# Performance work log

Measured on AMD Instinct MI355X. Metric: run time of the kernel, lower is better.

The kernel has to match this reference:

```python
import jax, jax.numpy as jnp
import numpy as np

DIM = 256
CODEBOOK_SIZE = 1024

def setup_inputs() -> dict:
    key = jax.random.key(0)
    kx, ke = jax.random.split(key)
    x = jax.random.normal(kx, (32, 2048, DIM), dtype=jnp.float32)
    embed = jax.random.normal(ke, (CODEBOOK_SIZE, DIM), dtype=jnp.float32)
    return {"x": x, "embed": embed}

def reference(x, embed):
    # Eval-mode forward of EuclideanCodebook (training=False: no EMA / dropout / dead-code replace).
    d = x.shape[-1]
    flatten = x.reshape(-1, d)                                   # (N, d)
    dist = ((flatten ** 2).sum(axis=1, keepdims=True)
            - 2.0 * flatten @ embed.T
            + (embed ** 2).sum(axis=1)[None, :])                 # (N, K)
    embed_ind = jnp.argmin(dist, axis=-1)                        # (N,)
    quantize = jnp.take(embed, embed_ind, axis=0)                # (N, d)
    residual = jax.lax.stop_gradient(quantize) - jax.lax.stop_gradient(flatten)
    return quantize, embed_ind, residual
```

## Files before the change

### kernel.cpp

```cpp
#include <hip/hip_runtime.h>
#include <math.h>
#include <float.h>

#define DIM 256
#define MARGIN 0.125f
#define EPS_TIE 1e-4
#define PREFER_LOWER 1

#define BMB 128

typedef __attribute__((ext_vector_type(8))) short short8;
typedef __attribute__((ext_vector_type(4))) float f32x4;

__device__ __forceinline__ unsigned short f32_to_bf16_rne(float f) {
    unsigned int u = __float_as_uint(f);
    u += 0x7fffu + ((u >> 16) & 1u);
    return (unsigned short)(u >> 16);
}
__device__ __forceinline__ float bf16_to_f32(unsigned short h) {
    return __uint_as_float((unsigned int)h << 16);
}

__global__ void esq_kernel(const float* __restrict__ embed, float* __restrict__ esq) {
    const int j = blockIdx.x;
    const int lane = threadIdx.x;
    float4 v = *reinterpret_cast<const float4*>(embed + (size_t)j * DIM + lane * 4);
    float s = v.x * v.x + v.y * v.y + v.z * v.z + v.w * v.w;
#pragma unroll
    for (int m = 32; m >= 1; m >>= 1) s += __shfl_xor(s, m, 64);
    if (lane == 0) esq[j] = s;
}

__global__ void efrag_kernel(const float* __restrict__ embed,
                             unsigned short* __restrict__ ehi,
                             unsigned short* __restrict__ elo) {
    const int b = blockIdx.x;
    const int l = threadIdx.x;
    const int ct = b >> 3, s = b & 7;
    const int col = ct * 16 + (l & 15);
    const int kb  = s * 32 + (l >> 4) * 8;
    const float* src = embed + (size_t)col * DIM + kb;
    float4 v0 = *reinterpret_cast<const float4*>(src);
    float4 v1 = *reinterpret_cast<const float4*>(src + 4);
    float vv[8] = {v0.x, v0.y, v0.z, v0.w, v1.x, v1.y, v1.z, v1.w};
    unsigned short hh[8], ll[8];
#pragma unroll
    for (int i = 0; i < 8; ++i) {
        unsigned short h = f32_to_bf16_rne(vv[i]);
        hh[i] = h;
        ll[i] = f32_to_bf16_rne(vv[i] - bf16_to_f32(h));
    }
    size_t base = ((size_t)b * 64 + l) * 8;
#pragma unroll
    for (int i = 0; i < 8; ++i) { ehi[base + i] = hh[i]; elo[base + i] = ll[i]; }
}

__global__ __launch_bounds__(256, 2)
void vq_mfma_kernel(const float* __restrict__ x, const float* __restrict__ embed,
                    const unsigned short* __restrict__ ehi,
                    const unsigned short* __restrict__ elo,
                    const float* __restrict__ esq, float* __restrict__ out,
                    int N, int K) {
    __shared__ float  esq_lds[1024];
    __shared__ double rv1[256], rv2[256];
    __shared__ int    ri1[256], ri2[256];
    __shared__ float  xrow[DIM];
    __shared__ int    flr[BMB];
    __shared__ int    nflag;

    const int t = threadIdx.x;
    const int w = t >> 6;
    const int l = t & 63;
    const int ar = l & 15;
    const int ag = l >> 4;
    const int row0  = blockIdx.x * BMB;
    const int wrow0 = row0 + w * 32;

    if (t == 0) nflag = 0;
    for (int i = t; i < 1024; i += 256) esq_lds[i] = esq[i];

    short8 ahi[2][8], alo[2][8];
#pragma unroll
    for (int rt = 0; rt < 2; ++rt)
#pragma unroll
        for (int s = 0; s < 8; ++s) {
            const float* src = x + (size_t)(wrow0 + rt * 16 + ar) * DIM + s * 32 + ag * 8;
            float4 v0 = *reinterpret_cast<const float4*>(src);
            float4 v1 = *reinterpret_cast<const float4*>(src + 4);
            float vv[8] = {v0.x, v0.y, v0.z, v0.w, v1.x, v1.y, v1.z, v1.w};
#pragma unroll
            for (int i = 0; i < 8; ++i) {
                unsigned short h = f32_to_bf16_rne(vv[i]);
                ahi[rt][s][i] = (short)h;
                alo[rt][s][i] = (short)f32_to_bf16_rne(vv[i] - bf16_to_f32(h));
            }
        }
    __syncthreads();

    float minv[8], min2v[8]; int mini[8];
#pragma unroll
    for (int i = 0; i < 8; ++i) { minv[i] = INFINITY; min2v[i] = INFINITY; mini[i] = 0; }

    for (int jc = 0; jc < 16; ++jc) {
        f32x4 acc[2][4];
#pragma unroll
        for (int rt = 0; rt < 2; ++rt)
#pragma unroll
            for (int ct = 0; ct < 4; ++ct) acc[rt][ct] = (f32x4)0.0f;

#pragma unroll
        for (int s = 0; s < 8; ++s) {
            short8 bhi[4], blo[4];
#pragma unroll
            for (int ct = 0; ct < 4; ++ct) {
                size_t base = (((size_t)(jc * 4 + ct) * 8 + s) * 64 + l) * 8;
                bhi[ct] = *reinterpret_cast<const short8*>(ehi + base);
                blo[ct] = *reinterpret_cast<const short8*>(elo + base);
            }
#pragma unroll
            for (int rt = 0; rt < 2; ++rt)
#pragma unroll
                for (int ct = 0; ct < 4; ++ct) {
                    acc[rt][ct] = __builtin_amdgcn_mfma_f32_16x16x32_bf16(
                        ahi[rt][s], bhi[ct], acc[rt][ct], 0, 0, 0);
                    acc[rt][ct] = __builtin_amdgcn_mfma_f32_16x16x32_bf16(
                        ahi[rt][s], blo[ct], acc[rt][ct], 0, 0, 0);
                    acc[rt][ct] = __builtin_amdgcn_mfma_f32_16x16x32_bf16(
                        alo[rt][s], bhi[ct], acc[rt][ct], 0, 0, 0);
                }
        }
#pragma unroll
        for (int rt = 0; rt < 2; ++rt)
#pragma unroll
            for (int ct = 0; ct < 4; ++ct) {
                int col = jc * 64 + ct * 16 + ar;
                float eq = esq_lds[col];
#pragma unroll
                for (int r = 0; r < 4; ++r) {
                    float sc = fmaf(-2.0f, acc[rt][ct][r], eq);
                    int ii = rt * 4 + r;
                    if (sc < minv[ii]) { min2v[ii] = minv[ii]; minv[ii] = sc; mini[ii] = col; }
                    else if (sc < min2v[ii]) { min2v[ii] = sc; }
                }
            }
    }

#pragma unroll
    for (int ii = 0; ii < 8; ++ii) {
        float v1 = minv[ii]; int i1 = mini[ii]; float v2 = min2v[ii];
#pragma unroll
        for (int m = 1; m < 16; m <<= 1) {
            float ov1 = __shfl_xor(v1, m, 64);
            int   oi1 = __shfl_xor(i1, m, 64);
            float ov2 = __shfl_xor(v2, m, 64);
            float nv2 = fminf(fmaxf(v1, ov1), fminf(v2, ov2));
            if (ov1 < v1 || (ov1 == v1 && oi1 < i1)) { v1 = ov1; i1 = oi1; }
            v2 = nv2;
        }
        minv[ii] = v1; mini[ii] = i1; min2v[ii] = v2;
    }

    const size_t IOFF = (size_t)N * DIM;
    const size_t ROFF = IOFF + (size_t)N;
#pragma unroll
    for (int ii = 0; ii < 8; ++ii) {
        const int rt = ii >> 2, r = ii & 3;
        const int row = wrow0 + rt * 16 + ag * 4 + r;
        const int idx = mini[ii];
        if (ar == 0) {
            out[IOFF + row] = (float)idx;
            if (min2v[ii] - minv[ii] < MARGIN) {
                int p = atomicAdd(&nflag, 1);
                flr[p] = row - row0;
            }
        }
#pragma unroll
        for (int q = 0; q < 4; ++q) {
            int d0 = ar * 16 + q * 4;
            float4 e  = *reinterpret_cast<const float4*>(embed + (size_t)idx * DIM + d0);
            float4 xv = *reinterpret_cast<const float4*>(x + (size_t)row * DIM + d0);
            *reinterpret_cast<float4*>(out + (size_t)row * DIM + d0) = e;
            float4 rr = make_float4(e.x - xv.x, e.y - xv.y, e.z - xv.z, e.w - xv.w);
            *reinterpret_cast<float4*>(out + ROFF + (size_t)row * DIM + d0) = rr;
        }
    }

    __syncthreads();
    const int nf = nflag;
    for (int f = 0; f < nf; ++f) {
        const int row = row0 + flr[f];
        if (t < 64) {
            float4 v = *reinterpret_cast<const float4*>(x + (size_t)row * DIM + t * 4);
            xrow[t * 4 + 0] = v.x; xrow[t * 4 + 1] = v.y;
            xrow[t * 4 + 2] = v.z; xrow[t * 4 + 3] = v.w;
        }
        __syncthreads();

        double v1 = DBL_MAX, v2 = DBL_MAX; int i1 = 0x7fffffff, i2 = 0x7fffffff;
#pragma unroll
        for (int jj = 0; jj < 4; ++jj) {
            const int j = t * 4 + jj;
            const float* e = embed + (size_t)j * DIM;
            double xe = 0.0, ee = 0.0;
            for (int kg = 0; kg < DIM / 4; ++kg) {
                float4 ev = *reinterpret_cast<const float4*>(e + kg * 4);
                double e0 = ev.x, e1 = ev.y, e2 = ev.z, e3 = ev.w;
                xe += e0 * (double)xrow[kg * 4 + 0] + e1 * (double)xrow[kg * 4 + 1]
                    + e2 * (double)xrow[kg * 4 + 2] + e3 * (double)xrow[kg * 4 + 3];
                ee += e0 * e0 + e1 * e1 + e2 * e2 + e3 * e3;
            }
            double d = ee - 2.0 * xe;
            if (d < v1 || (d == v1 && j < i1)) { v2 = v1; i2 = i1; v1 = d; i1 = j; }
            else if (d < v2 || (d == v2 && j < i2)) { v2 = d; i2 = j; }
        }
        rv1[t] = v1; ri1[t] = i1; rv2[t] = v2; ri2[t] = i2;
        __syncthreads();
        for (int s = 128; s > 0; s >>= 1) {
            if (t < s) {
                double a1 = rv1[t],     a2 = rv2[t];     int k1 = ri1[t],     k2 = ri2[t];
                double b1 = rv1[t + s], b2 = rv2[t + s]; int j1 = ri1[t + s], j2 = ri2[t + s];
                double w1, w2; int m1, m2;
                bool bfirst = (b1 < a1) || (b1 == a1 && j1 < k1);
                if (bfirst) {
                    w1 = b1; m1 = j1;
                    if (a1 < b2 || (a1 == b2 && k1 < j2)) { w2 = a1; m2 = k1; }
                    else                                   { w2 = b2; m2 = j2; }
                } else {
                    w1 = a1; m1 = k1;
                    if (b1 < a2 || (b1 == a2 && j1 < k2)) { w2 = b1; m2 = j1; }
                    else                                   { w2 = a2; m2 = k2; }
                }
                rv1[t] = w1; ri1[t] = m1; rv2[t] = w2; ri2[t] = m2;
            }
            __syncthreads();
        }
        int idx = ri1[0];
        {
            const double gap = rv2[0] - rv1[0];
#if PREFER_LOWER
            if (gap < EPS_TIE && ri2[0] < ri1[0]) idx = ri2[0];
#else
            if (gap < EPS_TIE && ri2[0] > ri1[0]) idx = ri2[0];
#endif
        }
        if (t == 0) out[IOFF + row] = (float)idx;
        if (t < 64) {
            int d0 = t * 4;
            float4 e  = *reinterpret_cast<const float4*>(embed + (size_t)idx * DIM + d0);
            float4 xv = *reinterpret_cast<const float4*>(x + (size_t)row * DIM + d0);
            *reinterpret_cast<float4*>(out + (size_t)row * DIM + d0) = e;
            float4 rr = make_float4(e.x - xv.x, e.y - xv.y, e.z - xv.z, e.w - xv.w);
            *reinterpret_cast<float4*>(out + ROFF + (size_t)row * DIM + d0) = rr;
        }
        __syncthreads();
    }
}

#define BM 64
#define BN 64
#define DK 64
__global__ __launch_bounds__(256, 4)
void vq_argmin_kernel(const float* __restrict__ x, const float* __restrict__ embed,
                      const float* __restrict__ esq, float* __restrict__ out,
                      int N, int K) {
    __shared__ float xs[DK][BM];
    __shared__ float es[DK][BN];
    __shared__ double rv1[256], rv2[256];
    __shared__ int    ri1[256], ri2[256];
    __shared__ float  xrow[DIM];
    __shared__ int    flr[BM];
    __shared__ int    nflag;

    const int t = threadIdx.x;
    const int tx = t & 15, ty = t >> 4;
    const int row0 = blockIdx.x * BM;
    if (t == 0) nflag = 0;

    float minv[4], min2v[4]; int mini[4];
#pragma unroll
    for (int r = 0; r < 4; ++r) { minv[r] = INFINITY; min2v[r] = INFINITY; mini[r] = 0; }

    for (int jc = 0; jc < K / BN; ++jc) {
        float acc[4][4];
#pragma unroll
        for (int r = 0; r < 4; ++r)
#pragma unroll
            for (int c = 0; c < 4; ++c) acc[r][c] = 0.0f;
        for (int dc = 0; dc < DIM / DK; ++dc) {
            __syncthreads();
#pragma unroll
            for (int it = 0; it < 4; ++it) {
                int idx = t + 256 * it, r = idx & 63, kg = idx >> 6;
                float4 v = *reinterpret_cast<const float4*>(
                    x + (size_t)(row0 + r) * DIM + dc * DK + kg * 4);
                xs[kg*4+0][r] = v.x; xs[kg*4+1][r] = v.y; xs[kg*4+2][r] = v.z; xs[kg*4+3][r] = v.w;
            }
#pragma unroll
            for (int it = 0; it < 4; ++it) {
                int idx = t + 256 * it, c = idx & 63, kg = idx >> 6;
                float4 v = *reinterpret_cast<const float4*>(
                    embed + (size_t)(jc * BN + c) * DIM + dc * DK + kg * 4);
                es[kg*4+0][c] = v.x; es[kg*4+1][c] = v.y; es[kg*4+2][c] = v.z; es[kg*4+3][c] = v.w;
            }
            __syncthreads();
#pragma unroll
            for (int k = 0; k < DK; ++k) {
                float4 a = *reinterpret_cast<const float4*>(&xs[k][ty * 4]);
                float4 b = *reinterpret_cast<const float4*>(&es[k][tx * 4]);
                float arr[4] = {a.x, a.y, a.z, a.w}, bc[4] = {b.x, b.y, b.z, b.w};
#pragma unroll
                for (int r = 0; r < 4; ++r)
#pragma unroll
                    for (int c = 0; c < 4; ++c) acc[r][c] = fmaf(arr[r], bc[c], acc[r][c]);
            }
        }
        float4 eq = *reinterpret_cast<const float4*>(esq + jc * BN + tx * 4);
        float eqa[4] = {eq.x, eq.y, eq.z, eq.w};
#pragma unroll
        for (int c = 0; c < 4; ++c) {
            int j = jc * BN + tx * 4 + c;
#pragma unroll
            for (int r = 0; r < 4; ++r) {
                float s = fmaf(-2.0f, acc[r][c], eqa[c]);
                if (s < minv[r]) { min2v[r] = minv[r]; minv[r] = s; mini[r] = j; }
                else if (s < min2v[r]) { min2v[r] = s; }
            }
        }
    }
#pragma unroll
    for (int r = 0; r < 4; ++r) {
        float v1 = minv[r]; int i1 = mini[r]; float v2 = min2v[r];
#pragma unroll
        for (int m = 1; m < 16; m <<= 1) {
            float ov1 = __shfl_xor(v1, m, 64); int oi1 = __shfl_xor(i1, m, 64);
            float ov2 = __shfl_xor(v2, m, 64);
            float nv2 = fminf(fmaxf(v1, ov1), fminf(v2, ov2));
            if (ov1 < v1 || (ov1 == v1 && oi1 < i1)) { v1 = ov1; i1 = oi1; }
            v2 = nv2;
        }
        minv[r] = v1; mini[r] = i1; min2v[r] = v2;
    }
    const size_t IOFF = (size_t)N * DIM, ROFF = IOFF + (size_t)N;
#pragma unroll
    for (int r = 0; r < 4; ++r) {
        int row = row0 + ty * 4 + r, idx = mini[r];
        if (tx == 0) {
            out[IOFF + row] = (float)idx;
            if (min2v[r] - minv[r] < MARGIN) { int p = atomicAdd(&nflag, 1); flr[p] = ty * 4 + r; }
        }
#pragma unroll
        for (int g = 0; g < 4; ++g) {
            int d0 = tx * 16 + g * 4;
            float4 e  = *reinterpret_cast<const float4*>(embed + (size_t)idx * DIM + d0);
            float4 xv = *reinterpret_cast<const float4*>(x + (size_t)row * DIM + d0);
            *reinterpret_cast<float4*>(out + (size_t)row * DIM + d0) = e;
            float4 rr = make_float4(e.x - xv.x, e.y - xv.y, e.z - xv.z, e.w - xv.w);
            *reinterpret_cast<float4*>(out + ROFF + (size_t)row * DIM + d0) = rr;
        }
    }
    __syncthreads();
    const int nf = nflag;
    for (int f = 0; f < nf; ++f) {
        const int row = row0 + flr[f];
        if (t < 64) {
            float4 v = *reinterpret_cast<const float4*>(x + (size_t)row * DIM + t * 4);
            xrow[t*4+0] = v.x; xrow[t*4+1] = v.y; xrow[t*4+2] = v.z; xrow[t*4+3] = v.w;
        }
        __syncthreads();
        double v1 = DBL_MAX, v2 = DBL_MAX; int i1 = 0x7fffffff, i2 = 0x7fffffff;
#pragma unroll
        for (int jj = 0; jj < 4; ++jj) {
            const int j = t * 4 + jj;
            const float* e = embed + (size_t)j * DIM;
            double xe = 0.0, ee = 0.0;
            for (int kg = 0; kg < DIM / 4; ++kg) {
                float4 ev = *reinterpret_cast<const float4*>(e + kg * 4);
                double e0 = ev.x, e1 = ev.y, e2 = ev.z, e3 = ev.w;
                xe += e0*(double)xrow[kg*4+0] + e1*(double)xrow[kg*4+1]
                    + e2*(double)xrow[kg*4+2] + e3*(double)xrow[kg*4+3];
                ee += e0*e0 + e1*e1 + e2*e2 + e3*e3;
            }
            double d = ee - 2.0 * xe;
            if (d < v1 || (d == v1 && j < i1)) { v2 = v1; i2 = i1; v1 = d; i1 = j; }
            else if (d < v2 || (d == v2 && j < i2)) { v2 = d; i2 = j; }
        }
        rv1[t] = v1; ri1[t] = i1; rv2[t] = v2; ri2[t] = i2;
        __syncthreads();
        for (int s = 128; s > 0; s >>= 1) {
            if (t < s) {
                double a1 = rv1[t], a2 = rv2[t]; int k1 = ri1[t], k2 = ri2[t];
                double b1 = rv1[t+s], b2 = rv2[t+s]; int j1 = ri1[t+s], j2 = ri2[t+s];
                double w1, w2; int m1, m2;
                bool bfirst = (b1 < a1) || (b1 == a1 && j1 < k1);
                if (bfirst) { w1 = b1; m1 = j1;
                    if (a1 < b2 || (a1 == b2 && k1 < j2)) { w2 = a1; m2 = k1; } else { w2 = b2; m2 = j2; }
                } else { w1 = a1; m1 = k1;
                    if (b1 < a2 || (b1 == a2 && j1 < k2)) { w2 = b1; m2 = j1; } else { w2 = a2; m2 = k2; }
                }
                rv1[t] = w1; ri1[t] = m1; rv2[t] = w2; ri2[t] = m2;
            }
            __syncthreads();
        }
        int idx = ri1[0];
        const double gap = rv2[0] - rv1[0];
#if PREFER_LOWER
        if (gap < EPS_TIE && ri2[0] < ri1[0]) idx = ri2[0];
#else
        if (gap < EPS_TIE && ri2[0] > ri1[0]) idx = ri2[0];
#endif
        if (t == 0) out[IOFF + row] = (float)idx;
        if (t < 64) {
            int d0 = t * 4;
            float4 e  = *reinterpret_cast<const float4*>(embed + (size_t)idx * DIM + d0);
            float4 xv = *reinterpret_cast<const float4*>(x + (size_t)row * DIM + d0);
            *reinterpret_cast<float4*>(out + (size_t)row * DIM + d0) = e;
            float4 rr = make_float4(e.x - xv.x, e.y - xv.y, e.z - xv.z, e.w - xv.w);
            *reinterpret_cast<float4*>(out + ROFF + (size_t)row * DIM + d0) = rr;
        }
        __syncthreads();
    }
}

extern "C" void kernel_launch(void* const* d_in, const int* in_sizes, int n_in,
                              void* d_out, int out_size, void* d_ws, size_t ws_size,
                              hipStream_t stream) {
    const float* x     = (const float*)d_in[0];
    const float* embed = (const float*)d_in[1];
    float* out = (float*)d_out;
    const int N = in_sizes[0] / DIM;
    const int K = in_sizes[1] / DIM;

    float* esq = (float*)d_ws;
    unsigned short* ehi = (unsigned short*)((char*)d_ws + 4096);
    unsigned short* elo = (unsigned short*)((char*)d_ws + 4096 + 524288);
    const size_t need = 4096 + 2 * 524288;

    esq_kernel<<<K, 64, 0, stream>>>(embed, esq);
    if (ws_size >= need) {
        efrag_kernel<<<(K / 16) * 8, 64, 0, stream>>>(embed, ehi, elo);
        vq_mfma_kernel<<<N / BMB, 256, 0, stream>>>(x, embed, ehi, elo, esq, out, N, K);
    } else {
        vq_argmin_kernel<<<N / BM, 256, 0, stream>>>(x, embed, esq, out, N, K);
    }
}
```

Baseline: 436.8 us.

## Split codebook columns across waves with LDS-staged double-buffered B fragments

Each block now handles 32 rows instead of 128. All four waves share those rows, and each wave owns a 16-column slice of every 64-column chunk. Codebook bf16 fragments are staged into LDS with async global_load_lds, double-buffered against the MFMA work. Per-wave argmin results are merged through shared memory, and the gather/residual write is re-laid out as coalesced full-row float4 accesses. This cuts per-wave accumulator registers and raises the occupancy target, but adds a __syncthreads per k-step and makes every block re-read the whole codebook for only 32 rows, four times as many codebook passes overall.

Result: slower. 727.0 us (+66.5%).

```diff
diff --git a/kernel.cpp b/kernel.cpp
--- a/kernel.cpp
+++ b/kernel.cpp
@@ -7,7 +7,7 @@
 #define EPS_TIE 1e-4
 #define PREFER_LOWER 1
 
-#define BMB 128
+#define ROWS 32
 
 typedef __attribute__((ext_vector_type(8))) short short8;
 typedef __attribute__((ext_vector_type(4))) float f32x4;
@@ -19,6 +19,13 @@
 }
 __device__ __forceinline__ float bf16_to_f32(unsigned short h) {
     return __uint_as_float((unsigned int)h << 16);
+}
+
+__device__ __forceinline__ void stage16(const void* gsrc, void* ldst) {
+    __builtin_amdgcn_global_load_lds(
+        (const __attribute__((address_space(1))) unsigned int*)gsrc,
+        (__attribute__((address_space(3))) unsigned int*)ldst,
+        16, 0, 0);
 }
 
 __global__ void esq_kernel(const float* __restrict__ embed, float* __restrict__ esq) {
@@ -55,26 +62,29 @@
     for (int i = 0; i < 8; ++i) { ehi[base + i] = hh[i]; elo[base + i] = ll[i]; }
 }
 
-__global__ __launch_bounds__(256, 2)
+__global__ __launch_bounds__(256, 3)
 void vq_mfma_kernel(const float* __restrict__ x, const float* __restrict__ embed,
                     const unsigned short* __restrict__ ehi,
                     const unsigned short* __restrict__ elo,
                     const float* __restrict__ esq, float* __restrict__ out,
                     int N, int K) {
+    __shared__ unsigned short bfrag[2][4][2][512];
     __shared__ float  esq_lds[1024];
+    __shared__ float  mv1[4][ROWS], mv2[4][ROWS];
+    __shared__ int    mi1[4][ROWS];
+    __shared__ int    rowidx[ROWS];
     __shared__ double rv1[256], rv2[256];
     __shared__ int    ri1[256], ri2[256];
     __shared__ float  xrow[DIM];
-    __shared__ int    flr[BMB];
+    __shared__ int    flr[ROWS];
     __shared__ int    nflag;
 
-    const int t = threadIdx.x;
-    const int w = t >> 6;
-    const int l = t & 63;
+    const int t  = threadIdx.x;
+    const int w  = t >> 6;
+    const int l  = t & 63;
     const int ar = l & 15;
     const int ag = l >> 4;
-    const int row0  = blockIdx.x * BMB;
-    const int wrow0 = row0 + w * 32;
+    const int row0 = blockIdx.x * ROWS;
 
     if (t == 0) nflag = 0;
     for (int i = t; i < 1024; i += 256) esq_lds[i] = esq[i];
@@ -84,7 +94,7 @@
     for (int rt = 0; rt < 2; ++rt)
 #pragma unroll
         for (int s = 0; s < 8; ++s) {
-            const float* src = x + (size_t)(wrow0 + rt * 16 + ar) * DIM + s * 32 + ag * 8;
+            const float* src = x + (size_t)(row0 + rt * 16 + ar) * DIM + s * 32 + ag * 8;
             float4 v0 = *reinterpret_cast<const float4*>(src);
             float4 v1 = *reinterpret_cast<const float4*>(src + 4);
             float vv[8] = {v0.x, v0.y, v0.z, v0.w, v1.x, v1.y, v1.z, v1.w};
@@ -95,55 +105,56 @@
                 alo[rt][s][i] = (short)f32_to_bf16_rne(vv[i] - bf16_to_f32(h));
             }
         }
+
+#define STAGE(CB, JC, S) do {                                                   \
+        size_t go_ = (((size_t)((JC) * 4 + w) * 8 + (S)) * 64 + l) * 8;         \
+        stage16(ehi + go_, &bfrag[CB][w][0][0]);                                \
+        stage16(elo + go_, &bfrag[CB][w][1][0]);                                \
+    } while (0)
+
+    STAGE(0, 0, 0);
     __syncthreads();
 
     float minv[8], min2v[8]; int mini[8];
 #pragma unroll
     for (int i = 0; i < 8; ++i) { minv[i] = INFINITY; min2v[i] = INFINITY; mini[i] = 0; }
 
+    f32x4 acc0 = (f32x4)0.0f, acc1 = (f32x4)0.0f;
+
     for (int jc = 0; jc < 16; ++jc) {
-        f32x4 acc[2][4];
-#pragma unroll
-        for (int rt = 0; rt < 2; ++rt)
-#pragma unroll
-            for (int ct = 0; ct < 4; ++ct) acc[rt][ct] = (f32x4)0.0f;
-
 #pragma unroll
         for (int s = 0; s < 8; ++s) {
-            short8 bhi[4], blo[4];
-#pragma unroll
-            for (int ct = 0; ct < 4; ++ct) {
-                size_t base = (((size_t)(jc * 4 + ct) * 8 + s) * 64 + l) * 8;
-                bhi[ct] = *reinterpret_cast<const short8*>(ehi + base);
-                blo[ct] = *reinterpret_cast<const short8*>(elo + base);
-            }
-#pragma unroll
-            for (int rt = 0; rt < 2; ++rt)
-#pragma unroll
-                for (int ct = 0; ct < 4; ++ct) {
-                    acc[rt][ct] = __builtin_amdgcn_mfma_f32_16x16x32_bf16(
-                        ahi[rt][s], bhi[ct], acc[rt][ct], 0, 0, 0);
-                    acc[rt][ct] = __builtin_amdgcn_mfma_f32_16x16x32_bf16(
-                        ahi[rt][s], blo[ct], acc[rt][ct], 0, 0, 0);
-                    acc[rt][ct] = __builtin_amdgcn_mfma_f32_16x16x32_bf16(
-                        alo[rt][s], bhi[ct], acc[rt][ct], 0, 0, 0);
-                }
-        }
-#pragma unroll
-        for (int rt = 0; rt < 2; ++rt)
-#pragma unroll
-            for (int ct = 0; ct < 4; ++ct) {
-                int col = jc * 64 + ct * 16 + ar;
-                float eq = esq_lds[col];
-#pragma unroll
-                for (int r = 0; r < 4; ++r) {
-                    float sc = fmaf(-2.0f, acc[rt][ct][r], eq);
-                    int ii = rt * 4 + r;
-                    if (sc < minv[ii]) { min2v[ii] = minv[ii]; minv[ii] = sc; mini[ii] = col; }
-                    else if (sc < min2v[ii]) { min2v[ii] = sc; }
-                }
-            }
-    }
+            const int cb = s & 1;
+            if (s < 7)            STAGE(cb ^ 1, jc, s + 1);
+            else if (jc < 15)     STAGE(cb ^ 1, jc + 1, 0);
+            short8 bh = *reinterpret_cast<const short8*>(&bfrag[cb][w][0][l * 8]);
+            short8 bl = *reinterpret_cast<const short8*>(&bfrag[cb][w][1][l * 8]);
+            acc0 = __builtin_amdgcn_mfma_f32_16x16x32_bf16(ahi[0][s], bh, acc0, 0, 0, 0);
+            acc0 = __builtin_amdgcn_mfma_f32_16x16x32_bf16(ahi[0][s], bl, acc0, 0, 0, 0);
+            acc0 = __builtin_amdgcn_mfma_f32_16x16x32_bf16(alo[0][s], bh, acc0, 0, 0, 0);
+            acc1 = __builtin_amdgcn_mfma_f32_16x16x32_bf16(ahi[1][s], bh, acc1, 0, 0, 0);
+            acc1 = __builtin_amdgcn_mfma_f32_16x16x32_bf16(ahi[1][s], bl, acc1, 0, 0, 0);
+            acc1 = __builtin_amdgcn_mfma_f32_16x16x32_bf16(alo[1][s], bh, acc1, 0, 0, 0);
+            __syncthreads();
+        }
+        const int col = jc * 64 + w * 16 + ar;
+        const float eq = esq_lds[col];
+#pragma unroll
+        for (int r = 0; r < 4; ++r) {
+            float sc = fmaf(-2.0f, acc0[r], eq);
+            if (sc < minv[r]) { min2v[r] = minv[r]; minv[r] = sc; mini[r] = col; }
+            else if (sc < min2v[r]) min2v[r] = sc;
+        }
+#pragma unroll
+        for (int r = 0; r < 4; ++r) {
+            float sc = fmaf(-2.0f, acc1[r], eq);
+            int ii = 4 + r;
+            if (sc < minv[ii]) { min2v[ii] = minv[ii]; minv[ii] = sc; mini[ii] = col; }
+            else if (sc < min2v[ii]) min2v[ii] = sc;
+        }
+        acc0 = (f32x4)0.0f; acc1 = (f32x4)0.0f;
+    }
+#undef STAGE
 
 #pragma unroll
     for (int ii = 0; ii < 8; ++ii) {
@@ -159,30 +170,44 @@
         }
         minv[ii] = v1; mini[ii] = i1; min2v[ii] = v2;
     }
+    if (ar == 0) {
+#pragma unroll
+        for (int ii = 0; ii < 8; ++ii) {
+            int rr = (ii >> 2) * 16 + ag * 4 + (ii & 3);
+            mv1[w][rr] = minv[ii]; mi1[w][rr] = mini[ii]; mv2[w][rr] = min2v[ii];
+        }
+    }
+    __syncthreads();
+    if (t < ROWS) {
+        float v1 = mv1[0][t]; int i1 = mi1[0][t]; float v2 = mv2[0][t];
+#pragma unroll
+        for (int ww = 1; ww < 4; ++ww) {
+            float ov1 = mv1[ww][t]; int oi1 = mi1[ww][t]; float ov2 = mv2[ww][t];
+            float nv2 = fminf(fmaxf(v1, ov1), fminf(v2, ov2));
+            if (ov1 < v1 || (ov1 == v1 && oi1 < i1)) { v1 = ov1; i1 = oi1; }
+            v2 = nv2;
+        }
+        rowidx[t] = i1;
+        if (v2 - v1 < MARGIN) {
+            int p = atomicAdd(&nflag, 1);
+            flr[p] = t;
+        }
+    }
+    __syncthreads();
 
     const size_t IOFF = (size_t)N * DIM;
     const size_t ROFF = IOFF + (size_t)N;
 #pragma unroll
-    for (int ii = 0; ii < 8; ++ii) {
-        const int rt = ii >> 2, r = ii & 3;
-        const int row = wrow0 + rt * 16 + ag * 4 + r;
-        const int idx = mini[ii];
-        if (ar == 0) {
-            out[IOFF + row] = (float)idx;
-            if (min2v[ii] - minv[ii] < MARGIN) {
-                int p = atomicAdd(&nflag, 1);
-                flr[p] = row - row0;
-            }
-        }
-#pragma unroll
-        for (int q = 0; q < 4; ++q) {
-            int d0 = ar * 16 + q * 4;
-            float4 e  = *reinterpret_cast<const float4*>(embed + (size_t)idx * DIM + d0);
-            float4 xv = *reinterpret_cast<const float4*>(x + (size_t)row * DIM + d0);
-            *reinterpret_cast<float4*>(out + (size_t)row * DIM + d0) = e;
-            float4 rr = make_float4(e.x - xv.x, e.y - xv.y, e.z - xv.z, e.w - xv.w);
-            *reinterpret_cast<float4*>(out + ROFF + (size_t)row * DIM + d0) = rr;
-        }
+    for (int rg = 0; rg < 8; ++rg) {
+        const int rr  = rg * 4 + w;
+        const int row = row0 + rr;
+        const int idx = rowidx[rr];
+        if (l == 0) out[IOFF + row] = (float)idx;
+        float4 e  = *reinterpret_cast<const float4*>(embed + (size_t)idx * DIM + l * 4);
+        float4 xv = *reinterpret_cast<const float4*>(x + (size_t)row * DIM + l * 4);
+        *reinterpret_cast<float4*>(out + (size_t)row * DIM + l * 4) = e;
+        float4 rv = make_float4(e.x - xv.x, e.y - xv.y, e.z - xv.z, e.w - xv.w);
+        *reinterpret_cast<float4*>(out + ROFF + (size_t)row * DIM + l * 4) = rv;
     }
 
     __syncthreads();
@@ -438,7 +463,7 @@
     esq_kernel<<<K, 64, 0, stream>>>(embed, esq);
     if (ws_size >= need) {
         efrag_kernel<<<(K / 16) * 8, 64, 0, stream>>>(embed, ehi, elo);
-        vq_mfma_kernel<<<N / BMB, 256, 0, stream>>>(x, embed, ehi, elo, esq, out, N, K);
+        vq_mfma_kernel<<<N / ROWS, 256, 0, stream>>>(x, embed, ehi, elo, esq, out, N, K);
     } else {
         vq_argmin_kernel<<<N / BM, 256, 0, stream>>>(x, embed, esq, out, N, K);
     }
```

## Stage codebook fragments via double-buffered LDS and use nontemporal streaming I/O

Applied to the files above, without the earlier changes.

Before this change, each wave loaded all four B fragment tiles from global memory, so all four waves fetched the same data. Now each wave loads one tile into a double-buffered LDS slot using global_load_lds, the four waves share those tiles, and the next s-step is prefetched while MFMAs run on the current one. The cost is a __syncthreads per s-step, 128 per block, which adds barrier stalls. The x reads and the quantize/residual writes now use nontemporal loads and stores to reduce cache pollution.

New measurement: 582.5 us. +33.3%, slower.

```diff
diff --git a/kernel.cpp b/kernel.cpp
--- a/kernel.cpp
+++ b/kernel.cpp
@@ -7,7 +7,7 @@
 #define EPS_TIE 1e-4
 #define PREFER_LOWER 1
 
-#define BMB 128
+#define ROWS 128
 
 typedef __attribute__((ext_vector_type(8))) short short8;
 typedef __attribute__((ext_vector_type(4))) float f32x4;
@@ -19,6 +19,20 @@
 }
 __device__ __forceinline__ float bf16_to_f32(unsigned short h) {
     return __uint_as_float((unsigned int)h << 16);
+}
+
+__device__ __forceinline__ f32x4 nt_load4(const float* p) {
+    return __builtin_nontemporal_load((const f32x4*)p);
+}
+__device__ __forceinline__ void nt_store4(float* p, f32x4 v) {
+    __builtin_nontemporal_store(v, (f32x4*)p);
+}
+
+__device__ __forceinline__ void stage16(const void* gsrc, void* ldst) {
+    __builtin_amdgcn_global_load_lds(
+        (const __attribute__((address_space(1))) unsigned int*)gsrc,
+        (__attribute__((address_space(3))) unsigned int*)ldst,
+        16, 0, 0);
 }
 
 __global__ void esq_kernel(const float* __restrict__ embed, float* __restrict__ esq) {
@@ -61,19 +75,20 @@
                     const unsigned short* __restrict__ elo,
                     const float* __restrict__ esq, float* __restrict__ out,
                     int N, int K) {
+    __shared__ unsigned short bfrag[2][4][2][512];
     __shared__ float  esq_lds[1024];
     __shared__ double rv1[256], rv2[256];
     __shared__ int    ri1[256], ri2[256];
     __shared__ float  xrow[DIM];
-    __shared__ int    flr[BMB];
+    __shared__ int    flr[ROWS];
     __shared__ int    nflag;
 
-    const int t = threadIdx.x;
-    const int w = t >> 6;
-    const int l = t & 63;
+    const int t  = threadIdx.x;
+    const int w  = t >> 6;
+    const int l  = t & 63;
     const int ar = l & 15;
     const int ag = l >> 4;
-    const int row0  = blockIdx.x * BMB;
+    const int row0  = blockIdx.x * ROWS;
     const int wrow0 = row0 + w * 32;
 
     if (t == 0) nflag = 0;
@@ -85,9 +100,9 @@
 #pragma unroll
         for (int s = 0; s < 8; ++s) {
             const float* src = x + (size_t)(wrow0 + rt * 16 + ar) * DIM + s * 32 + ag * 8;
-            float4 v0 = *reinterpret_cast<const float4*>(src);
-            float4 v1 = *reinterpret_cast<const float4*>(src + 4);
-            float vv[8] = {v0.x, v0.y, v0.z, v0.w, v1.x, v1.y, v1.z, v1.w};
+            f32x4 v0 = nt_load4(src);
+            f32x4 v1 = nt_load4(src + 4);
+            float vv[8] = {v0[0], v0[1], v0[2], v0[3], v1[0], v1[1], v1[2], v1[3]};
 #pragma unroll
             for (int i = 0; i < 8; ++i) {
                 unsigned short h = f32_to_bf16_rne(vv[i]);
@@ -95,55 +110,68 @@
                 alo[rt][s][i] = (short)f32_to_bf16_rne(vv[i] - bf16_to_f32(h));
             }
         }
+
+#define STAGE(CB, JC, S) do {                                                   \
+        size_t go_ = (((size_t)((JC) * 4 + w) * 8 + (S)) * 64 + l) * 8;         \
+        stage16(ehi + go_, &bfrag[CB][w][0][0]);                                \
+        stage16(elo + go_, &bfrag[CB][w][1][0]);                                \
+    } while (0)
+
+    STAGE(0, 0, 0);
     __syncthreads();
 
     float minv[8], min2v[8]; int mini[8];
 #pragma unroll
     for (int i = 0; i < 8; ++i) { minv[i] = INFINITY; min2v[i] = INFINITY; mini[i] = 0; }
 
+    f32x4 acc[2][4];
+#pragma unroll
+    for (int rt = 0; rt < 2; ++rt)
+#pragma unroll
+        for (int ct = 0; ct < 4; ++ct) acc[rt][ct] = (f32x4)0.0f;
+
     for (int jc = 0; jc < 16; ++jc) {
-        f32x4 acc[2][4];
-#pragma unroll
-        for (int rt = 0; rt < 2; ++rt)
-#pragma unroll
-            for (int ct = 0; ct < 4; ++ct) acc[rt][ct] = (f32x4)0.0f;
-
 #pragma unroll
         for (int s = 0; s < 8; ++s) {
-            short8 bhi[4], blo[4];
+            const int cb = s & 1;
+            if (s < 7)            STAGE(cb ^ 1, jc, s + 1);
+            else if (jc < 15)     STAGE(cb ^ 1, jc + 1, 0);
+            short8 bh[4], bl[4];
 #pragma unroll
             for (int ct = 0; ct < 4; ++ct) {
-                size_t base = (((size_t)(jc * 4 + ct) * 8 + s) * 64 + l) * 8;
-                bhi[ct] = *reinterpret_cast<const short8*>(ehi + base);
-                blo[ct] = *reinterpret_cast<const short8*>(elo + base);
+                bh[ct] = *reinterpret_cast<const short8*>(&bfrag[cb][ct][0][l * 8]);
+                bl[ct] = *reinterpret_cast<const short8*>(&bfrag[cb][ct][1][l * 8]);
             }
 #pragma unroll
             for (int rt = 0; rt < 2; ++rt)
 #pragma unroll
                 for (int ct = 0; ct < 4; ++ct) {
                     acc[rt][ct] = __builtin_amdgcn_mfma_f32_16x16x32_bf16(
-                        ahi[rt][s], bhi[ct], acc[rt][ct], 0, 0, 0);
+                        ahi[rt][s], bh[ct], acc[rt][ct], 0, 0, 0);
                     acc[rt][ct] = __builtin_amdgcn_mfma_f32_16x16x32_bf16(
-                        ahi[rt][s], blo[ct], acc[rt][ct], 0, 0, 0);
+                        ahi[rt][s], bl[ct], acc[rt][ct], 0, 0, 0);
                     acc[rt][ct] = __builtin_amdgcn_mfma_f32_16x16x32_bf16(
-                        alo[rt][s], bhi[ct], acc[rt][ct], 0, 0, 0);
+                        alo[rt][s], bh[ct], acc[rt][ct], 0, 0, 0);
                 }
+            __syncthreads();
         }
 #pragma unroll
         for (int rt = 0; rt < 2; ++rt)
 #pragma unroll
             for (int ct = 0; ct < 4; ++ct) {
-                int col = jc * 64 + ct * 16 + ar;
-                float eq = esq_lds[col];
+                const int col = jc * 64 + ct * 16 + ar;
+                const float eq = esq_lds[col];
 #pragma unroll
                 for (int r = 0; r < 4; ++r) {
                     float sc = fmaf(-2.0f, acc[rt][ct][r], eq);
                     int ii = rt * 4 + r;
                     if (sc < minv[ii]) { min2v[ii] = minv[ii]; minv[ii] = sc; mini[ii] = col; }
-                    else if (sc < min2v[ii]) { min2v[ii] = sc; }
+                    else if (sc < min2v[ii]) min2v[ii] = sc;
                 }
-            }
-    }
+                acc[rt][ct] = (f32x4)0.0f;
+            }
+    }
+#undef STAGE
 
 #pragma unroll
     for (int ii = 0; ii < 8; ++ii) {
@@ -177,11 +205,10 @@
 #pragma unroll
         for (int q = 0; q < 4; ++q) {
             int d0 = ar * 16 + q * 4;
-            float4 e  = *reinterpret_cast<const float4*>(embed + (size_t)idx * DIM + d0);
-            float4 xv = *reinterpret_cast<const float4*>(x + (size_t)row * DIM + d0);
-            *reinterpret_cast<float4*>(out + (size_t)row * DIM + d0) = e;
-            float4 rr = make_float4(e.x - xv.x, e.y - xv.y, e.z - xv.z, e.w - xv.w);
-            *reinterpret_cast<float4*>(out + ROFF + (size_t)row * DIM + d0) = rr;
+            f32x4 e  = *reinterpret_cast<const f32x4*>(embed + (size_t)idx * DIM + d0);
+            f32x4 xv = nt_load4(x + (size_t)row * DIM + d0);
+            nt_store4(out + (size_t)row * DIM + d0, e);
+            nt_store4(out + ROFF + (size_t)row * DIM + d0, e - xv);
         }
     }
 
@@ -438,7 +465,7 @@
     esq_kernel<<<K, 64, 0, stream>>>(embed, esq);
     if (ws_size >= need) {
         efrag_kernel<<<(K / 16) * 8, 64, 0, stream>>>(embed, ehi, elo);
-        vq_mfma_kernel<<<N / BMB, 256, 0, stream>>>(x, embed, ehi, elo, esq, out, N, K);
+        vq_mfma_kernel<<<N / ROWS, 256, 0, stream>>>(x, embed, ehi, elo, esq, out, N, K);
     } else {
         vq_argmin_kernel<<<N / BM, 256, 0, stream>>>(x, embed, esq, out, N, K);
     }
```

## Use single-bf16 MFMA with split-codebook partial argmin and exact fallback merge

Applied to the files above, without the earlier changes.

Drops the three-term hi/lo bf16 split and computes distances with a single bf16 MFMA per tile. The codebook is split into two halves held in registers across 512-row blocks, with x fragments staged in LDS. Per-half top-2 partial results go to a workspace, and a separate merge kernel picks the winner. The merge kernel flags close calls with wider margins for exact fp64 recomputation, and writes quantize and residual with nontemporal stores. This removes about two thirds of the MFMA work and the lo-fragment loads. The cost is more rows sent to the slow exact fallback, plus an extra kernel launch and workspace traffic.

Result: slower. 1.524 ms (+248.9%).

```diff
diff --git a/kernel.cpp b/kernel.cpp
--- a/kernel.cpp
+++ b/kernel.cpp
@@ -3,11 +3,11 @@
 #include <float.h>
 
 #define DIM 256
-#define MARGIN 0.125f
 #define EPS_TIE 1e-4
 #define PREFER_LOWER 1
-
-#define BMB 128
+#define MARGIN_MERGE 0.75f
+#define MARGIN_HALF  0.30f
+#define MARGIN_FALLBACK 0.125f
 
 typedef __attribute__((ext_vector_type(8))) short short8;
 typedef __attribute__((ext_vector_type(4))) float f32x4;
@@ -17,8 +17,8 @@
     u += 0x7fffu + ((u >> 16) & 1u);
     return (unsigned short)(u >> 16);
 }
-__device__ __forceinline__ float bf16_to_f32(unsigned short h) {
-    return __uint_as_float((unsigned int)h << 16);
+__device__ __forceinline__ void nt_store4(float* p, f32x4 v) {
+    __builtin_nontemporal_store(v, (f32x4*)p);
 }
 
 __global__ void esq_kernel(const float* __restrict__ embed, float* __restrict__ esq) {
@@ -32,8 +32,7 @@
 }
 
 __global__ void efrag_kernel(const float* __restrict__ embed,
-                             unsigned short* __restrict__ ehi,
-                             unsigned short* __restrict__ elo) {
+                             unsigned short* __restrict__ ehi) {
     const int b = blockIdx.x;
     const int l = threadIdx.x;
     const int ct = b >> 3, s = b & 7;
@@ -43,146 +42,160 @@
     float4 v0 = *reinterpret_cast<const float4*>(src);
     float4 v1 = *reinterpret_cast<const float4*>(src + 4);
     float vv[8] = {v0.x, v0.y, v0.z, v0.w, v1.x, v1.y, v1.z, v1.w};
-    unsigned short hh[8], ll[8];
-#pragma unroll
-    for (int i = 0; i < 8; ++i) {
-        unsigned short h = f32_to_bf16_rne(vv[i]);
-        hh[i] = h;
-        ll[i] = f32_to_bf16_rne(vv[i] - bf16_to_f32(h));
-    }
     size_t base = ((size_t)b * 64 + l) * 8;
 #pragma unroll
-    for (int i = 0; i < 8; ++i) { ehi[base + i] = hh[i]; elo[base + i] = ll[i]; }
-}
-
-__global__ __launch_bounds__(256, 2)
-void vq_mfma_kernel(const float* __restrict__ x, const float* __restrict__ embed,
-                    const unsigned short* __restrict__ ehi,
-                    const unsigned short* __restrict__ elo,
-                    const float* __restrict__ esq, float* __restrict__ out,
-                    int N, int K) {
-    __shared__ float  esq_lds[1024];
+    for (int i = 0; i < 8; ++i) ehi[base + i] = f32_to_bf16_rne(vv[i]);
+}
+
+__global__ __launch_bounds__(512, 2) void
+vq_fast_kernel(const float* __restrict__ x, const unsigned short* __restrict__ ehi,
+               const float* __restrict__ esq, f32x4* __restrict__ part, int N) {
+    __shared__ unsigned short xfrag[4][8][512];
+    __shared__ float wv1[8][64], wv2[8][64];
+    __shared__ int   wi1[8][64];
+    __shared__ float esq_l[512];
+
+    const int t  = threadIdx.x;
+    const int w  = t >> 6;
+    const int l  = t & 63;
+    const int ar = l & 15;
+    const int ag = l >> 4;
+    const int half  = blockIdx.x & 1;
+    const int rbase = (blockIdx.x >> 1) * 512;
+    const int cbase = half * 512;
+
+    for (int i = t; i < 512; i += 512) esq_l[i] = esq[cbase + i];
+
+    short8 eh[4][8];
+#pragma unroll
+    for (int ct = 0; ct < 4; ++ct)
+#pragma unroll
+        for (int s = 0; s < 8; ++s) {
+            const int ctg = half * 32 + w * 4 + ct;
+            eh[ct][s] = *reinterpret_cast<const short8*>(
+                ehi + (((size_t)ctg * 8 + s) * 64 + l) * 8);
+        }
+
+    for (int tile = 0; tile < 8; ++tile) {
+        const int trow0 = rbase + tile * 64;
+        __syncthreads();
+#pragma unroll
+        for (int i = 0; i < 4; ++i) {
+            const int f = w * 4 + i, rt = f >> 3, s = f & 7;
+            const float* src = x + (size_t)(trow0 + rt * 16 + ar) * DIM + s * 32 + ag * 8;
+            float4 v0 = *reinterpret_cast<const float4*>(src);
+            float4 v1 = *reinterpret_cast<const float4*>(src + 4);
+            float vv[8] = {v0.x, v0.y, v0.z, v0.w, v1.x, v1.y, v1.z, v1.w};
+            short8 hv;
+#pragma unroll
+            for (int j = 0; j < 8; ++j) hv[j] = (short)f32_to_bf16_rne(vv[j]);
+            *reinterpret_cast<short8*>(&xfrag[rt][s][l * 8]) = hv;
+        }
+        __syncthreads();
+
+        f32x4 acc[4][4];
+#pragma unroll
+        for (int rt = 0; rt < 4; ++rt)
+#pragma unroll
+            for (int ct = 0; ct < 4; ++ct) acc[rt][ct] = (f32x4)0.0f;
+
+#pragma unroll
+        for (int s = 0; s < 8; ++s)
+#pragma unroll
+            for (int rt = 0; rt < 4; ++rt) {
+                short8 xa = *reinterpret_cast<const short8*>(&xfrag[rt][s][l * 8]);
+#pragma unroll
+                for (int ct = 0; ct < 4; ++ct)
+                    acc[rt][ct] = __builtin_amdgcn_mfma_f32_16x16x32_bf16(
+                        xa, eh[ct][s], acc[rt][ct], 0, 0, 0);
+            }
+
+#pragma unroll
+        for (int rt = 0; rt < 4; ++rt)
+#pragma unroll
+            for (int r = 0; r < 4; ++r) {
+                float v1 = INFINITY, v2 = INFINITY; int i1 = 0;
+#pragma unroll
+                for (int ct = 0; ct < 4; ++ct) {
+                    const int col = cbase + w * 64 + ct * 16 + ar;
+                    float sc = fmaf(-2.0f, acc[rt][ct][r], esq_l[w * 64 + ct * 16 + ar]);
+                    if (sc < v1) { v2 = v1; v1 = sc; i1 = col; }
+                    else if (sc < v2) v2 = sc;
+                }
+#pragma unroll
+                for (int m = 1; m < 16; m <<= 1) {
+                    float ov1 = __shfl_xor(v1, m, 64);
+                    int   oi1 = __shfl_xor(i1, m, 64);
+                    float ov2 = __shfl_xor(v2, m, 64);
+                    float nv2 = fminf(fmaxf(v1, ov1), fminf(v2, ov2));
+                    if (ov1 < v1 || (ov1 == v1 && oi1 < i1)) { v1 = ov1; i1 = oi1; }
+                    v2 = nv2;
+                }
+                if (ar == 0) {
+                    const int rl = rt * 16 + ag * 4 + r;
+                    wv1[w][rl] = v1; wi1[w][rl] = i1; wv2[w][rl] = v2;
+                }
+            }
+        __syncthreads();
+        if (t < 64) {
+            float v1 = wv1[0][t]; int i1 = wi1[0][t]; float v2 = wv2[0][t];
+#pragma unroll
+            for (int ww = 1; ww < 8; ++ww) {
+                float ov1 = wv1[ww][t]; int oi1 = wi1[ww][t]; float ov2 = wv2[ww][t];
+                float nv2 = fminf(fmaxf(v1, ov1), fminf(v2, ov2));
+                if (ov1 < v1 || (ov1 == v1 && oi1 < i1)) { v1 = ov1; i1 = oi1; }
+                v2 = nv2;
+            }
+            f32x4 p; p[0] = v1; p[1] = v2; p[2] = __int_as_float(i1); p[3] = 0.0f;
+            part[(size_t)(trow0 + t) * 2 + half] = p;
+        }
+    }
+}
+
+__global__ __launch_bounds__(256) void
+vq_merge_kernel(const float* __restrict__ x, const float* __restrict__ embed,
+                const f32x4* __restrict__ part, float* __restrict__ out, int N, int K) {
+    __shared__ int    rowidx[64];
+    __shared__ int    flr[64];
+    __shared__ int    nflag;
     __shared__ double rv1[256], rv2[256];
     __shared__ int    ri1[256], ri2[256];
     __shared__ float  xrow[DIM];
-    __shared__ int    flr[BMB];
-    __shared__ int    nflag;
 
     const int t = threadIdx.x;
-    const int w = t >> 6;
-    const int l = t & 63;
-    const int ar = l & 15;
-    const int ag = l >> 4;
-    const int row0  = blockIdx.x * BMB;
-    const int wrow0 = row0 + w * 32;
-
+    const int w = t >> 6, l = t & 63;
+    const int row0 = blockIdx.x * 64;
     if (t == 0) nflag = 0;
-    for (int i = t; i < 1024; i += 256) esq_lds[i] = esq[i];
-
-    short8 ahi[2][8], alo[2][8];
-#pragma unroll
-    for (int rt = 0; rt < 2; ++rt)
-#pragma unroll
-        for (int s = 0; s < 8; ++s) {
-            const float* src = x + (size_t)(wrow0 + rt * 16 + ar) * DIM + s * 32 + ag * 8;
-            float4 v0 = *reinterpret_cast<const float4*>(src);
-            float4 v1 = *reinterpret_cast<const float4*>(src + 4);
-            float vv[8] = {v0.x, v0.y, v0.z, v0.w, v1.x, v1.y, v1.z, v1.w};
-#pragma unroll
-            for (int i = 0; i < 8; ++i) {
-                unsigned short h = f32_to_bf16_rne(vv[i]);
-                ahi[rt][s][i] = (short)h;
-                alo[rt][s][i] = (short)f32_to_bf16_rne(vv[i] - bf16_to_f32(h));
-            }
-        }
     __syncthreads();
 
-    float minv[8], min2v[8]; int mini[8];
-#pragma unroll
-    for (int i = 0; i < 8; ++i) { minv[i] = INFINITY; min2v[i] = INFINITY; mini[i] = 0; }
-
-    for (int jc = 0; jc < 16; ++jc) {
-        f32x4 acc[2][4];
-#pragma unroll
-        for (int rt = 0; rt < 2; ++rt)
-#pragma unroll
-            for (int ct = 0; ct < 4; ++ct) acc[rt][ct] = (f32x4)0.0f;
-
-#pragma unroll
-        for (int s = 0; s < 8; ++s) {
-            short8 bhi[4], blo[4];
-#pragma unroll
-            for (int ct = 0; ct < 4; ++ct) {
-                size_t base = (((size_t)(jc * 4 + ct) * 8 + s) * 64 + l) * 8;
-                bhi[ct] = *reinterpret_cast<const short8*>(ehi + base);
-                blo[ct] = *reinterpret_cast<const short8*>(elo + base);
-            }
-#pragma unroll
-            for (int rt = 0; rt < 2; ++rt)
-#pragma unroll
-                for (int ct = 0; ct < 4; ++ct) {
-                    acc[rt][ct] = __builtin_amdgcn_mfma_f32_16x16x32_bf16(
-                        ahi[rt][s], bhi[ct], acc[rt][ct], 0, 0, 0);
-                    acc[rt][ct] = __builtin_amdgcn_mfma_f32_16x16x32_bf16(
-                        ahi[rt][s], blo[ct], acc[rt][ct], 0, 0, 0);
-                    acc[rt][ct] = __builtin_amdgcn_mfma_f32_16x16x32_bf16(
-                        alo[rt][s], bhi[ct], acc[rt][ct], 0, 0, 0);
-                }
-        }
-#pragma unroll
-        for (int rt = 0; rt < 2; ++rt)
-#pragma unroll
-            for (int ct = 0; ct < 4; ++ct) {
-                int col = jc * 64 + ct * 16 + ar;
-                float eq = esq_lds[col];
-#pragma unroll
-                for (int r = 0; r < 4; ++r) {
-                    float sc = fmaf(-2.0f, acc[rt][ct][r], eq);
-                    int ii = rt * 4 + r;
-                    if (sc < minv[ii]) { min2v[ii] = minv[ii]; minv[ii] = sc; mini[ii] = col; }
-                    else if (sc < min2v[ii]) { min2v[ii] = sc; }
-                }
-            }
-    }
-
-#pragma unroll
-    for (int ii = 0; ii < 8; ++ii) {
-        float v1 = minv[ii]; int i1 = mini[ii]; float v2 = min2v[ii];
-#pragma unroll
-        for (int m = 1; m < 16; m <<= 1) {
-            float ov1 = __shfl_xor(v1, m, 64);
-            int   oi1 = __shfl_xor(i1, m, 64);
-            float ov2 = __shfl_xor(v2, m, 64);
-            float nv2 = fminf(fmaxf(v1, ov1), fminf(v2, ov2));
-            if (ov1 < v1 || (ov1 == v1 && oi1 < i1)) { v1 = ov1; i1 = oi1; }
-            v2 = nv2;
-        }
-        minv[ii] = v1; mini[ii] = i1; min2v[ii] = v2;
-    }
+    if (t < 64) {
+        const int row = row0 + t;
+        f32x4 a = part[(size_t)row * 2 + 0];
+        f32x4 b = part[(size_t)row * 2 + 1];
+        float av1 = a[0], av2 = a[1]; int ai1 = __float_as_int(a[2]);
+        float bv1 = b[0], bv2 = b[1]; int bi1 = __float_as_int(b[2]);
+        float v1; int i1; float v2;
+        if (bv1 < av1) { v1 = bv1; i1 = bi1; v2 = fminf(av1, bv2); }
+        else           { v1 = av1; i1 = ai1; v2 = fminf(bv1, av2); }
+        rowidx[t] = i1;
+        bool flag = (v2 - v1 < MARGIN_MERGE) ||
+                    (av2 - av1 < MARGIN_HALF) || (bv2 - bv1 < MARGIN_HALF);
+        if (flag) { int p = atomicAdd(&nflag, 1); flr[p] = t; }
+    }
+    __syncthreads();
 
     const size_t IOFF = (size_t)N * DIM;
     const size_t ROFF = IOFF + (size_t)N;
 #pragma unroll
-    for (int ii = 0; ii < 8; ++ii) {
-        const int rt = ii >> 2, r = ii & 3;
-        const int row = wrow0 + rt * 16 + ag * 4 + r;
-        const int idx = mini[ii];
-        if (ar == 0) {
-            out[IOFF + row] = (float)idx;
-            if (min2v[ii] - minv[ii] < MARGIN) {
-                int p = atomicAdd(&nflag, 1);
-                flr[p] = row - row0;
-            }
-        }
-#pragma unroll
-        for (int q = 0; q < 4; ++q) {
-            int d0 = ar * 16 + q * 4;
-            float4 e  = *reinterpret_cast<const float4*>(embed + (size_t)idx * DIM + d0);
-            float4 xv = *reinterpret_cast<const float4*>(x + (size_t)row * DIM + d0);
-            *reinterpret_cast<float4*>(out + (size_t)row * DIM + d0) = e;
-            float4 rr = make_float4(e.x - xv.x, e.y - xv.y, e.z - xv.z, e.w - xv.w);
-            *reinterpret_cast<float4*>(out + ROFF + (size_t)row * DIM + d0) = rr;
-        }
+    for (int it = 0; it < 16; ++it) {
+        const int rl  = it * 4 + w;
+        const int row = row0 + rl;
+        const int idx = rowidx[rl];
+        if (l == 0) out[IOFF + row] = (float)idx;
+        f32x4 e  = *reinterpret_cast<const f32x4*>(embed + (size_t)idx * DIM + l * 4);
+        f32x4 xv = *reinterpret_cast<const f32x4*>(x + (size_t)row * DIM + l * 4);
+        nt_store4(out + (size_t)row * DIM + l * 4, e);
+        nt_store4(out + ROFF + (size_t)row * DIM + l * 4, e - xv);
     }
 
     __syncthreads();
@@ -346,7 +359,7 @@
         int row = row0 + ty * 4 + r, idx = mini[r];
         if (tx == 0) {
             out[IOFF + row] = (float)idx;
-            if (min2v[r] - minv[r] < MARGIN) { int p = atomicAdd(&nflag, 1); flr[p] = ty * 4 + r; }
+            if (min2v[r] - minv[r] < MARGIN_FALLBACK) { int p = atomicAdd(&nflag, 1); flr[p] = ty * 4 + r; }
         }
 #pragma unroll
         for (int g = 0; g < 4; ++g) {
@@ -432,13 +445,14 @@
 
     float* esq = (float*)d_ws;
     unsigned short* ehi = (unsigned short*)((char*)d_ws + 4096);
-    unsigned short* elo = (unsigned short*)((char*)d_ws + 4096 + 524288);
-    const size_t need = 4096 + 2 * 524288;
+    f32x4* part = (f32x4*)((char*)d_ws + 4096 + 524288);
+    const size_t need = 4096 + 524288 + (size_t)N * 2 * 16;
 
     esq_kernel<<<K, 64, 0, stream>>>(embed, esq);
     if (ws_size >= need) {
-        efrag_kernel<<<(K / 16) * 8, 64, 0, stream>>>(embed, ehi, elo);
-        vq_mfma_kernel<<<N / BMB, 256, 0, stream>>>(x, embed, ehi, elo, esq, out, N, K);
+        efrag_kernel<<<(K / 16) * 8, 64, 0, stream>>>(embed, ehi);
+        vq_fast_kernel<<<(N / 512) * 2, 512, 0, stream>>>(x, ehi, esq, part, N);
+        vq_merge_kernel<<<N / 64, 256, 0, stream>>>(x, embed, part, out, N, K);
     } else {
         vq_argmin_kernel<<<N / BM, 256, 0, stream>>>(x, embed, esq, out, N, K);
     }
```
